# Kernel tuning notes

Measured on AMD Instinct MI355X. Metric: run time of the kernel, lower is better.

The kernel has to match this reference:

```python
import jax, jax.numpy as jnp
import numpy as np

NIN = 128
NUM_CLASSES = 3
NUM_FC = 3
SUB_STEPS = 2
SUB_POINTS = 8192


def setup_inputs() -> dict:
    key = jax.random.key(0)
    ks = jax.random.split(key, 8)
    N, H, W = 4, 128, 128
    inp = {
        'coarse_sem_seg_logits': jax.random.normal(ks[0], (N, NUM_CLASSES, H, W), jnp.float32),
        'features': jax.random.normal(ks[1], (N, NIN, 2 * H, 2 * W), jnp.float32),
    }
    fan_in = NIN + NUM_CLASSES  # coarse preds concatenated at every layer
    for i in range(NUM_FC):
        # kaiming normal fan_out for conv1d(k=1): std = sqrt(2 / out_channels)
        inp[f'w{i+1}'] = jax.random.normal(ks[2 + i], (NIN, fan_in), jnp.float32) * np.sqrt(2.0 / NIN)
        inp[f'b{i+1}'] = jnp.zeros((NIN,), jnp.float32)
    inp['wp'] = jax.random.normal(ks[5], (NUM_CLASSES, NIN + NUM_CLASSES), jnp.float32) * 0.001
    inp['bp'] = jnp.zeros((NUM_CLASSES,), jnp.float32)
    return inp


def point_sample(feat, pc):
    """Bilinear sample feat (N,C,H,W) at normalized coords pc (N,P,2) in [0,1]^2.
    Matches torch grid_sample(2*pc-1, mode='bilinear', align_corners=False, padding='zeros').
    pixel = coord * size - 0.5 (half-pixel centers)."""
    N, C, H, W = feat.shape
    x = pc[..., 0] * W - 0.5  # (N,P)
    y = pc[..., 1] * H - 0.5
    x0 = jnp.floor(x)
    y0 = jnp.floor(y)
    x0i = x0.astype(jnp.int32)
    y0i = y0.astype(jnp.int32)
    wx1 = x - x0
    wy1 = y - y0

    def corner(xi, yi, w):
        valid = ((xi >= 0) & (xi < W) & (yi >= 0) & (yi < H)).astype(feat.dtype)
        xc = jnp.clip(xi, 0, W - 1)
        yc = jnp.clip(yi, 0, H - 1)
        gather = jax.vmap(lambda f, yy, xx: f[:, yy, xx])  # (C,H,W),(P,),(P,) -> (C,P)
        vals = gather(feat, yc, xc)  # (N,C,P)
        return vals * (w * valid)[:, None, :]

    return (corner(x0i, y0i, (1 - wx1) * (1 - wy1))
            + corner(x0i + 1, y0i, wx1 * (1 - wy1))
            + corner(x0i, y0i + 1, (1 - wx1) * wy1)
            + corner(x0i + 1, y0i + 1, wx1 * wy1))


def calc_uncertainty(logits):
    # logits (N,C,H,W), C>1: uncertainty = top2 - top1 (<=0, highest = most uncertain)
    t = jnp.moveaxis(logits, 1, -1)  # (N,H,W,C)
    top2 = jax.lax.top_k(t, 2)[0]
    return top2[..., 1] - top2[..., 0]  # (N,H,W)


def bilinear_up2(x):
    N, C, H, W = x.shape
    return jax.image.resize(x, (N, C, 2 * H, 2 * W), method='bilinear')


def reference(coarse_sem_seg_logits, features, w1, b1, w2, b2, w3, b3, wp, bp):
    fc = [(w1, b1), (w2, b2), (w3, b3)]

    def point_head(fine, coarse):
        # conv1d with kernel 1 == per-point matmul; coarse preds re-concatenated each layer
        x = jnp.concatenate([fine, coarse], axis=1)  # (N,Cin,P)
        for w, b in fc:
            x = jax.nn.relu(jnp.einsum('oi,nip->nop', w, x) + b[None, :, None])
            x = jnp.concatenate([x, coarse], axis=1)
        return jnp.einsum('oi,nip->nop', wp, x) + bp[None, :, None]

    sem = coarse_sem_seg_logits
    for _ in range(SUB_STEPS):
        sem = bilinear_up2(sem)
        N, C, H, W = sem.shape
        unc = calc_uncertainty(sem).reshape(N, H * W)
        P = min(H * W, SUB_POINTS)
        idx = jax.lax.top_k(unc, P)[1]  # (N,P) most-uncertain grid points
        px = (idx % W + 0.5) / W
        py = (idx // W + 0.5) / H
        pc = jnp.stack([px, py], axis=-1).astype(sem.dtype)  # (N,P,2)
        coarse_pts = point_sample(coarse_sem_seg_logits, pc)  # (N,C,P)
        fine_pts = point_sample(features, pc)                 # (N,nin,P)
        point_logits = point_head(fine_pts, coarse_pts)       # (N,C,P)
        flat = sem.reshape(N, C, H * W)
        flat = flat.at[jnp.arange(N)[:, None, None],
                       jnp.arange(C)[None, :, None],
                       idx[:, None, :]].set(point_logits)
        sem = flat.reshape(N, C, H, W)
    return sem
```

## Files before the change

kernel.cpp:

```cpp
#include <hip/hip_runtime.h>
#include <stdint.h>

#define PSEL 8192
#define PB 32

static __device__ __forceinline__ uint32_t fkey(float f) {
    uint32_t u = __float_as_uint(f);
    return (u & 0x80000000u) ? ~u : (u | 0x80000000u);
}
static __device__ __forceinline__ uint64_t make_key(uint32_t k32, uint32_t idx) {
    return ((uint64_t)k32 << 18) | (uint64_t)(0x3FFFFu ^ idx);
}

__global__ void pr_up(const float* __restrict__ in, float* __restrict__ out,
                      uint32_t* __restrict__ keys, int Hc, int Wc,
                      uint64_t* __restrict__ prefix, uint32_t* __restrict__ krem,
                      uint32_t* __restrict__ cnt) {
    const int H = Hc * 2, W = Wc * 2, HW = H * W;
    int gid = blockIdx.x * blockDim.x + threadIdx.x;
    if (gid < 4) { prefix[gid] = 0ull; krem[gid] = PSEL; cnt[gid] = 0u; }
    if (gid >= 4 * HW) return;
    int w = gid % W;
    int t = gid / W;
    int h = t % H;
    int n = t / H;
    int kx = w >> 1, ky = h >> 1;
    int xlo, xhi, ylo, yhi; float wxl, wxh, wyl, wyh;
    if (w & 1) { xlo = kx; xhi = kx + 1; wxl = 0.75f; wxh = 0.25f; if (xhi >= Wc) { xhi = xlo; wxl = 1.0f; wxh = 0.0f; } }
    else       { xlo = kx - 1; xhi = kx; wxl = 0.25f; wxh = 0.75f; if (xlo < 0)  { xlo = xhi; wxl = 0.0f; wxh = 1.0f; } }
    if (h & 1) { ylo = ky; yhi = ky + 1; wyl = 0.75f; wyh = 0.25f; if (yhi >= Hc) { yhi = ylo; wyl = 1.0f; wyh = 0.0f; } }
    else       { ylo = ky - 1; yhi = ky; wyl = 0.25f; wyh = 0.75f; if (ylo < 0)  { ylo = yhi; wyl = 0.0f; wyh = 1.0f; } }
    float s0 = 0.f, s1 = 0.f, s2 = 0.f;
    #pragma unroll
    for (int c = 0; c < 3; c++) {
        const float* p = in + ((n * 3 + c) * Hc) * Wc;
        float tlo = wyl * p[ylo * Wc + xlo] + wyh * p[yhi * Wc + xlo];
        float thi = wyl * p[ylo * Wc + xhi] + wyh * p[yhi * Wc + xhi];
        float v = wxl * tlo + wxh * thi;
        out[((n * 3 + c) * H + h) * W + w] = v;
        if (c == 0) s0 = v; else if (c == 1) s1 = v; else s2 = v;
    }
    float m01 = fmaxf(s0, s1), mn01 = fminf(s0, s1);
    float mx = fmaxf(m01, s2);
    float sec = (s2 > m01) ? m01 : fmaxf(mn01, s2);
    keys[n * HW + h * W + w] = fkey(sec - mx);
}

__global__ void pr_hist(const uint32_t* __restrict__ keys, const uint64_t* __restrict__ prefix,
                        uint32_t* __restrict__ hist, int HW, int shift) {
    __shared__ uint32_t lh[1024];
    const int n = blockIdx.y;
    for (int i = threadIdx.x; i < 1024; i += blockDim.x) lh[i] = 0u;
    __syncthreads();
    uint64_t pref = prefix[n];
    const uint32_t* kp = keys + (size_t)n * HW;
    int stride = gridDim.x * blockDim.x;
    for (int i = blockIdx.x * blockDim.x + threadIdx.x; i < HW; i += stride) {
        uint64_t key = make_key(kp[i], (uint32_t)i);
        if ((key >> (shift + 10)) == pref)
            atomicAdd(&lh[(uint32_t)(key >> shift) & 1023u], 1u);
    }
    __syncthreads();
    for (int i = threadIdx.x; i < 1024; i += blockDim.x) {
        uint32_t v = lh[i];
        if (v) atomicAdd(&hist[n * 1024 + i], v);
    }
}

__global__ __launch_bounds__(256) void pr_scan(uint32_t* __restrict__ hist, uint64_t* __restrict__ prefix,
                                               uint32_t* __restrict__ krem, uint64_t* __restrict__ thr,
                                               int last) {
    const int n = blockIdx.x;
    const int t = threadIdx.x;
    __shared__ uint32_t h[1024];
    __shared__ uint32_t csum[256];
    __shared__ int sel_d;
    __shared__ uint32_t sel_above;
    uint32_t* hp = hist + n * 1024;
    uint32_t h0 = hp[t * 4 + 0], h1 = hp[t * 4 + 1], h2 = hp[t * 4 + 2], h3 = hp[t * 4 + 3];
    h[t * 4 + 0] = h0; h[t * 4 + 1] = h1; h[t * 4 + 2] = h2; h[t * 4 + 3] = h3;
    uint32_t s = h0 + h1 + h2 + h3;
    csum[t] = s;
    __syncthreads();
    for (int off = 1; off < 256; off <<= 1) {
        uint32_t add = (t + off < 256) ? csum[t + off] : 0u;
        __syncthreads();
        csum[t] += add;
        __syncthreads();
    }
    uint32_t krm = krem[n];
    uint32_t run = csum[t] - s;
    for (int b = 3; b >= 0; b--) {
        uint32_t hv = h[t * 4 + b];
        if (run < krm && krm <= run + hv) { sel_d = t * 4 + b; sel_above = run; }
        run += hv;
    }
    __syncthreads();
    if (t == 0) {
        uint64_t np = (prefix[n] << 10) | (uint64_t)(uint32_t)sel_d;
        prefix[n] = np;
        krem[n] = krm - sel_above;
        if (last) thr[n] = np;
    }
    hp[t * 4 + 0] = 0u; hp[t * 4 + 1] = 0u; hp[t * 4 + 2] = 0u; hp[t * 4 + 3] = 0u;
}

__global__ __launch_bounds__(256) void pr_compact(const uint32_t* __restrict__ keys,
                                                  const uint64_t* __restrict__ thr,
                                                  uint32_t* __restrict__ cnt,
                                                  uint32_t* __restrict__ pts, int HW) {
    __shared__ uint32_t lbuf[4096];
    __shared__ uint32_t lcnt, gbase;
    const int n = blockIdx.y;
    const int t = threadIdx.x;
    if (t == 0) lcnt = 0u;
    __syncthreads();
    uint64_t T = thr[n];
    const uint32_t* kp = keys + (size_t)n * HW;
    int stride = gridDim.x * blockDim.x;
    for (int i = blockIdx.x * blockDim.x + t; i < HW; i += stride) {
        uint64_t key = make_key(kp[i], (uint32_t)i);
        if (key >= T) {
            uint32_t p = atomicAdd(&lcnt, 1u);
            if (p < 4096u) lbuf[p] = (uint32_t)i;
        }
    }
    __syncthreads();
    if (t == 0) gbase = atomicAdd(&cnt[n], lcnt);
    __syncthreads();
    uint32_t m = lcnt;
    uint32_t gb = gbase;
    for (uint32_t j = t; j < m; j += 256u) {
        uint32_t pos = gb + j;
        if (pos < PSEL) pts[n * PSEL + pos] = lbuf[j];
    }
}

__global__ __launch_bounds__(256) void pr_mlp2(
        const float* __restrict__ feat, const float* __restrict__ coarse,
        const float* __restrict__ w1, const float* __restrict__ b1,
        const float* __restrict__ w2, const float* __restrict__ b2,
        const float* __restrict__ w3, const float* __restrict__ b3,
        const float* __restrict__ wp, const float* __restrict__ bp,
        const uint32_t* __restrict__ pts, float* __restrict__ sem, int W) {
    __shared__ __align__(16) float xbuf[131 * 36];
    __shared__ float wchunk[128 * 33];
    __shared__ uint32_t ptl[PB];
    const int t = threadIdx.x;
    const int n = blockIdx.y;
    if (t < PB) ptl[t] = pts[n * PSEL + blockIdx.x * PB + t];
    __syncthreads();
    const int lw = (W == 512) ? 9 : 8;
    {
        const int pt = t & 31, csl = t >> 5;
        uint32_t idx = ptl[pt];
        int ix = (int)(idx & (uint32_t)(W - 1));
        int iy = (int)(idx >> lw);
        const float* fb = feat + (size_t)n * 128 * 65536;
        if (W == 256) {
            const float* p0 = fb + (size_t)(csl * 16) * 65536 + iy * 256 + ix;
            #pragma unroll 4
            for (int k = 0; k < 16; k++)
                xbuf[(csl * 16 + k) * 36 + pt] = p0[(size_t)k * 65536];
        } else {
            float px = ((float)ix + 0.5f) / (float)W;
            float py = ((float)iy + 0.5f) / (float)W;
            float fx = px * 256.0f - 0.5f, fy = py * 256.0f - 0.5f;
            float x0f = floorf(fx), y0f = floorf(fy);
            int x0 = (int)x0f, y0 = (int)y0f;
            float wx1 = fx - x0f, wy1 = fy - y0f;
            float wx0 = 1.0f - wx1, wy0 = 1.0f - wy1;
            int x1 = x0 + 1, y1 = y0 + 1;
            float vx0 = (x0 >= 0 && x0 < 256) ? 1.0f : 0.0f;
            float vx1 = (x1 >= 0 && x1 < 256) ? 1.0f : 0.0f;
            float vy0 = (y0 >= 0 && y0 < 256) ? 1.0f : 0.0f;
            float vy1 = (y1 >= 0 && y1 < 256) ? 1.0f : 0.0f;
            int xc0 = min(max(x0, 0), 255), xc1 = min(max(x1, 0), 255);
            int yc0 = min(max(y0, 0), 255), yc1 = min(max(y1, 0), 255);
            int o00 = yc0 * 256 + xc0, o01 = yc0 * 256 + xc1;
            int o10 = yc1 * 256 + xc0, o11 = yc1 * 256 + xc1;
            float w00 = (wx0 * wy0) * (vx0 * vy0), w01 = (wx1 * wy0) * (vx1 * vy0);
            float w10 = (wx0 * wy1) * (vx0 * vy1), w11 = (wx1 * wy1) * (vx1 * vy1);
            const float* p0 = fb + (size_t)(csl * 16) * 65536;
            #pragma unroll 2
            for (int k = 0; k < 16; k++) {
                const float* p = p0 + (size_t)k * 65536;
                float v = p[o00] * w00 + p[o01] * w01 + p[o10] * w10 + p[o11] * w11;
                xbuf[(csl * 16 + k) * 36 + pt] = v;
            }
        }
    }
    if (t < 96) {
        const int pt = t & 31, cc = t >> 5;
        uint32_t idx = ptl[pt];
        int ix = (int)(idx & (uint32_t)(W - 1));
        int iy = (int)(idx >> lw);
        float px = ((float)ix + 0.5f) / (float)W;
        float py = ((float)iy + 0.5f) / (float)W;
        float gx = px * 128.0f - 0.5f, gy = py * 128.0f - 0.5f;
        float x0f = floorf(gx), y0f = floorf(gy);
        int x0 = (int)x0f, y0 = (int)y0f;
        float u1 = gx - x0f, v1 = gy - y0f;
        float u0 = 1.0f - u1, v0 = 1.0f - v1;
        int x1 = x0 + 1, y1 = y0 + 1;
        float vx0 = (x0 >= 0 && x0 < 128) ? 1.0f : 0.0f;
        float vx1 = (x1 >= 0 && x1 < 128) ? 1.0f : 0.0f;
        float vy0 = (y0 >= 0 && y0 < 128) ? 1.0f : 0.0f;
        float vy1 = (y1 >= 0 && y1 < 128) ? 1.0f : 0.0f;
        int xc0 = min(max(x0, 0), 127), xc1 = min(max(x1, 0), 127);
        int yc0 = min(max(y0, 0), 127), yc1 = min(max(y1, 0), 127);
        const float* cb = coarse + ((size_t)(n * 3 + cc)) * 16384;
        float v = cb[yc0 * 128 + xc0] * ((u0 * v0) * (vx0 * vy0))
                + cb[yc0 * 128 + xc1] * ((u1 * v0) * (vx1 * vy0))
                + cb[yc1 * 128 + xc0] * ((u0 * v1) * (vx0 * vy1))
                + cb[yc1 * 128 + xc1] * ((u1 * v1) * (vx1 * vy1));
        xbuf[(128 + cc) * 36 + pt] = v;
    }
    __syncthreads();
    const int o2 = t & 63, ph = t >> 6;
    float accA[8], accB[8];

    auto layer = [&](const float* __restrict__ Wg, const float* __restrict__ Bg) {
        float bA = Bg[o2], bB = Bg[o2 + 64];
        #pragma unroll
        for (int j = 0; j < 8; j++) { accA[j] = bA; accB[j] = bB; }
        for (int i0 = 0; i0 < 128; i0 += 32) {
            __syncthreads();
            for (int j = t; j < 4096; j += 256) {
                int o = j >> 5, ii = j & 31;
                wchunk[o * 33 + ii] = Wg[o * 131 + i0 + ii];
            }
            __syncthreads();
            #pragma unroll
            for (int ii = 0; ii < 32; ii++) {
                float wA = wchunk[o2 * 33 + ii];
                float wB = wchunk[(o2 + 64) * 33 + ii];
                const float4* xr = (const float4*)&xbuf[(i0 + ii) * 36 + ph * 8];
                float4 xv0 = xr[0], xv1 = xr[1];
                accA[0] = fmaf(wA, xv0.x, accA[0]); accA[1] = fmaf(wA, xv0.y, accA[1]);
                accA[2] = fmaf(wA, xv0.z, accA[2]); accA[3] = fmaf(wA, xv0.w, accA[3]);
                accA[4] = fmaf(wA, xv1.x, accA[4]); accA[5] = fmaf(wA, xv1.y, accA[5]);
                accA[6] = fmaf(wA, xv1.z, accA[6]); accA[7] = fmaf(wA, xv1.w, accA[7]);
                accB[0] = fmaf(wB, xv0.x, accB[0]); accB[1] = fmaf(wB, xv0.y, accB[1]);
                accB[2] = fmaf(wB, xv0.z, accB[2]); accB[3] = fmaf(wB, xv0.w, accB[3]);
                accB[4] = fmaf(wB, xv1.x, accB[4]); accB[5] = fmaf(wB, xv1.y, accB[5]);
                accB[6] = fmaf(wB, xv1.z, accB[6]); accB[7] = fmaf(wB, xv1.w, accB[7]);
            }
        }
        __syncthreads();
        for (int j = t; j < 384; j += 256) {
            int o = j / 3, ii = j - o * 3;
            wchunk[o * 33 + ii] = Wg[o * 131 + 128 + ii];
        }
        __syncthreads();
        #pragma unroll
        for (int ii = 0; ii < 3; ii++) {
            float wA = wchunk[o2 * 33 + ii];
            float wB = wchunk[(o2 + 64) * 33 + ii];
            const float4* xr = (const float4*)&xbuf[(128 + ii) * 36 + ph * 8];
            float4 xv0 = xr[0], xv1 = xr[1];
            accA[0] = fmaf(wA, xv0.x, accA[0]); accA[1] = fmaf(wA, xv0.y, accA[1]);
            accA[2] = fmaf(wA, xv0.z, accA[2]); accA[3] = fmaf(wA, xv0.w, accA[3]);
            accA[4] = fmaf(wA, xv1.x, accA[4]); accA[5] = fmaf(wA, xv1.y, accA[5]);
            accA[6] = fmaf(wA, xv1.z, accA[6]); accA[7] = fmaf(wA, xv1.w, accA[7]);
            accB[0] = fmaf(wB, xv0.x, accB[0]); accB[1] = fmaf(wB, xv0.y, accB[1]);
            accB[2] = fmaf(wB, xv0.z, accB[2]); accB[3] = fmaf(wB, xv0.w, accB[3]);
            accB[4] = fmaf(wB, xv1.x, accB[4]); accB[5] = fmaf(wB, xv1.y, accB[5]);
            accB[6] = fmaf(wB, xv1.z, accB[6]); accB[7] = fmaf(wB, xv1.w, accB[7]);
        }
        __syncthreads();
        #pragma unroll
        for (int j = 0; j < 8; j++) {
            xbuf[o2 * 36 + ph * 8 + j] = fmaxf(accA[j], 0.0f);
            xbuf[(o2 + 64) * 36 + ph * 8 + j] = fmaxf(accB[j], 0.0f);
        }
    };
    layer(w1, b1);
    layer(w2, b2);
    layer(w3, b3);
    __syncthreads();
    if (t < 96) {
        int cc = t >> 5, pt = t & 31;
        float acc = bp[cc];
        const float* wr = wp + cc * 131;
        for (int i = 0; i < 131; i++)
            acc = fmaf(wr[i], xbuf[i * 36 + pt], acc);
        sem[((size_t)(n * 3 + cc)) * W * W + ptl[pt]] = acc;
    }
}

extern "C" void kernel_launch(void* const* d_in, const int* in_sizes, int n_in,
                              void* d_out, int out_size, void* d_ws, size_t ws_size,
                              hipStream_t stream) {
    const float* coarse = (const float*)d_in[0];
    const float* feat   = (const float*)d_in[1];
    const float* w1 = (const float*)d_in[2];
    const float* b1 = (const float*)d_in[3];
    const float* w2 = (const float*)d_in[4];
    const float* b2 = (const float*)d_in[5];
    const float* w3 = (const float*)d_in[6];
    const float* b3 = (const float*)d_in[7];
    const float* wp = (const float*)d_in[8];
    const float* bp = (const float*)d_in[9];
    float* out = (float*)d_out;

    char* base = (char*)d_ws;
    float*    sem1   = (float*)base;
    uint32_t* keys   = (uint32_t*)(base + 3145728);
    uint32_t* hist   = (uint32_t*)(base + 7340032);
    uint64_t* prefix = (uint64_t*)(base + 7356416);
    uint64_t* thr    = (uint64_t*)(base + 7356448);
    uint32_t* krem   = (uint32_t*)(base + 7356480);
    uint32_t* cnt    = (uint32_t*)(base + 7356496);
    uint32_t* pts    = (uint32_t*)(base + 7356512);
    if (ws_size < (size_t)7487584) return;

    hipMemsetAsync(hist, 0, 4 * 1024 * sizeof(uint32_t), stream);

    for (int step = 0; step < 2; step++) {
        const float* sin_ = (step == 0) ? coarse : sem1;
        float* sout = (step == 0) ? sem1 : out;
        int Hc = (step == 0) ? 128 : 256;
        int H = 2 * Hc, HW = H * H;
        int total = 4 * HW;
        pr_up<<<dim3((total + 255) / 256), dim3(256), 0, stream>>>(
            sin_, sout, keys, Hc, Hc, prefix, krem, cnt);
        for (int p = 0; p < 5; p++) {
            int shift = 40 - 10 * p;
            pr_hist<<<dim3(16, 4), dim3(256), 0, stream>>>(keys, prefix, hist, HW, shift);
            pr_scan<<<dim3(4), dim3(256), 0, stream>>>(hist, prefix, krem, thr, p == 4 ? 1 : 0);
        }
        pr_compact<<<dim3(64, 4), dim3(256), 0, stream>>>(keys, thr, cnt, pts, HW);
        pr_mlp2<<<dim3(PSEL / PB, 4), dim3(256), 0, stream>>>(
            feat, coarse, w1, b1, w2, b2, w3, b3, wp, bp, pts, sout, H);
    }
}
```

Before: 541.6 us.

## Replace atomic compaction with deterministic count-scan-emit selection

The single atomic-based compaction kernel is replaced by three kernels: a per-block count of selected keys, a scan of block counts, and an emit pass that writes indices in sorted order using per-thread contiguous ranges. This makes the point order deterministic and removes shared and global atomics. In exchange it adds two extra launches, reads the keys twice, and uses strided per-thread access (each thread handles a contiguous chunk), which coalesces poorly.

```diff
diff --git a/kernel.cpp b/kernel.cpp
--- a/kernel.cpp
+++ b/kernel.cpp
@@ -14,11 +14,10 @@
 
 __global__ void pr_up(const float* __restrict__ in, float* __restrict__ out,
                       uint32_t* __restrict__ keys, int Hc, int Wc,
-                      uint64_t* __restrict__ prefix, uint32_t* __restrict__ krem,
-                      uint32_t* __restrict__ cnt) {
+                      uint64_t* __restrict__ prefix, uint32_t* __restrict__ krem) {
     const int H = Hc * 2, W = Wc * 2, HW = H * W;
     int gid = blockIdx.x * blockDim.x + threadIdx.x;
-    if (gid < 4) { prefix[gid] = 0ull; krem[gid] = PSEL; cnt[gid] = 0u; }
+    if (gid < 4) { prefix[gid] = 0ull; krem[gid] = PSEL; }
     if (gid >= 4 * HW) return;
     int w = gid % W;
     int t = gid / W;
@@ -105,34 +104,76 @@
     hp[t * 4 + 0] = 0u; hp[t * 4 + 1] = 0u; hp[t * 4 + 2] = 0u; hp[t * 4 + 3] = 0u;
 }
 
-__global__ __launch_bounds__(256) void pr_compact(const uint32_t* __restrict__ keys,
-                                                  const uint64_t* __restrict__ thr,
-                                                  uint32_t* __restrict__ cnt,
-                                                  uint32_t* __restrict__ pts, int HW) {
-    __shared__ uint32_t lbuf[4096];
-    __shared__ uint32_t lcnt, gbase;
-    const int n = blockIdx.y;
+__global__ __launch_bounds__(256) void pr_count(const uint32_t* __restrict__ keys,
+                                                const uint64_t* __restrict__ thr,
+                                                uint32_t* __restrict__ bcnt, int HW) {
+    __shared__ uint32_t red[256];
+    const int n = blockIdx.y, b = blockIdx.x, t = threadIdx.x;
+    const int per = HW >> 14;
+    const uint64_t T = thr[n];
+    const uint32_t* kp = keys + (size_t)n * HW;
+    int start = (b * 256 + t) * per;
+    uint32_t c = 0;
+    for (int k = 0; k < per; k++) {
+        int i = start + k;
+        c += (make_key(kp[i], (uint32_t)i) >= T) ? 1u : 0u;
+    }
+    red[t] = c;
+    __syncthreads();
+    for (int off = 128; off > 0; off >>= 1) {
+        if (t < off) red[t] += red[t + off];
+        __syncthreads();
+    }
+    if (t == 0) bcnt[n * 64 + b] = red[0];
+}
+
+__global__ __launch_bounds__(256) void pr_bscan(const uint32_t* __restrict__ bcnt,
+                                                uint32_t* __restrict__ bbase) {
+    __shared__ uint32_t s[256];
     const int t = threadIdx.x;
-    if (t == 0) lcnt = 0u;
-    __syncthreads();
-    uint64_t T = thr[n];
+    uint32_t v = bcnt[t];
+    s[t] = v;
+    __syncthreads();
+    for (int off = 1; off < 64; off <<= 1) {
+        uint32_t add = ((t & 63) >= off) ? s[t - off] : 0u;
+        __syncthreads();
+        s[t] += add;
+        __syncthreads();
+    }
+    bbase[t] = s[t] - v;
+}
+
+__global__ __launch_bounds__(256) void pr_emit(const uint32_t* __restrict__ keys,
+                                               const uint64_t* __restrict__ thr,
+                                               const uint32_t* __restrict__ bbase,
+                                               uint32_t* __restrict__ pts, int HW) {
+    __shared__ uint32_t s[256];
+    const int n = blockIdx.y, b = blockIdx.x, t = threadIdx.x;
+    const int per = HW >> 14;
+    const uint64_t T = thr[n];
     const uint32_t* kp = keys + (size_t)n * HW;
-    int stride = gridDim.x * blockDim.x;
-    for (int i = blockIdx.x * blockDim.x + t; i < HW; i += stride) {
-        uint64_t key = make_key(kp[i], (uint32_t)i);
-        if (key >= T) {
-            uint32_t p = atomicAdd(&lcnt, 1u);
-            if (p < 4096u) lbuf[p] = (uint32_t)i;
-        }
-    }
-    __syncthreads();
-    if (t == 0) gbase = atomicAdd(&cnt[n], lcnt);
-    __syncthreads();
-    uint32_t m = lcnt;
-    uint32_t gb = gbase;
-    for (uint32_t j = t; j < m; j += 256u) {
-        uint32_t pos = gb + j;
-        if (pos < PSEL) pts[n * PSEL + pos] = lbuf[j];
+    int start = (b * 256 + t) * per;
+    uint32_t c = 0;
+    for (int k = 0; k < per; k++) {
+        int i = start + k;
+        c += (make_key(kp[i], (uint32_t)i) >= T) ? 1u : 0u;
+    }
+    s[t] = c;
+    __syncthreads();
+    for (int off = 1; off < 256; off <<= 1) {
+        uint32_t add = (t >= off) ? s[t - off] : 0u;
+        __syncthreads();
+        s[t] += add;
+        __syncthreads();
+    }
+    uint32_t pos = bbase[n * 64 + b] + s[t] - c;
+    uint32_t* pp = pts + n * PSEL;
+    for (int k = 0; k < per; k++) {
+        int i = start + k;
+        if (make_key(kp[i], (uint32_t)i) >= T) {
+            if (pos < PSEL) pp[pos] = (uint32_t)i;
+            pos++;
+        }
     }
 }
 
@@ -311,9 +352,10 @@
     uint64_t* prefix = (uint64_t*)(base + 7356416);
     uint64_t* thr    = (uint64_t*)(base + 7356448);
     uint32_t* krem   = (uint32_t*)(base + 7356480);
-    uint32_t* cnt    = (uint32_t*)(base + 7356496);
     uint32_t* pts    = (uint32_t*)(base + 7356512);
-    if (ws_size < (size_t)7487584) return;
+    uint32_t* bcnt   = (uint32_t*)(base + 7487584);
+    uint32_t* bbase  = (uint32_t*)(base + 7488608);
+    if (ws_size < (size_t)7489632) return;
 
     hipMemsetAsync(hist, 0, 4 * 1024 * sizeof(uint32_t), stream);
 
@@ -324,13 +366,15 @@
         int H = 2 * Hc, HW = H * H;
         int total = 4 * HW;
         pr_up<<<dim3((total + 255) / 256), dim3(256), 0, stream>>>(
-            sin_, sout, keys, Hc, Hc, prefix, krem, cnt);
+            sin_, sout, keys, Hc, Hc, prefix, krem);
         for (int p = 0; p < 5; p++) {
             int shift = 40 - 10 * p;
             pr_hist<<<dim3(16, 4), dim3(256), 0, stream>>>(keys, prefix, hist, HW, shift);
             pr_scan<<<dim3(4), dim3(256), 0, stream>>>(hist, prefix, krem, thr, p == 4 ? 1 : 0);
         }
-        pr_compact<<<dim3(64, 4), dim3(256), 0, stream>>>(keys, thr, cnt, pts, HW);
+        pr_count<<<dim3(64, 4), dim3(256), 0, stream>>>(keys, thr, bcnt, HW);
+        pr_bscan<<<dim3(1), dim3(256), 0, stream>>>(bcnt, bbase);
+        pr_emit<<<dim3(64, 4), dim3(256), 0, stream>>>(keys, thr, bbase, pts, HW);
         pr_mlp2<<<dim3(PSEL / PB, 4), dim3(256), 0, stream>>>(
             feat, coarse, w1, b1, w2, b2, w3, b3, wp, bp, pts, sout, H);
     }
```

New measurement: 537.3 us. No clear change (-0.8%).
